# Optimization experiments

Hardware: AMD Instinct MI355X
Metric: run time of the kernel (lower is better)

The kernel has to match this reference:

```python
import jax, jax.numpy as jnp
import numpy as np

NQ = 4        # nqubits
NLAYERS = 2   # nlayers
DIM = 2 ** NQ # statevector size = 16


def _apply_1q(state, U, wire, batched):
    """Apply a single-qubit gate U on `wire` to state [B, 16].
    U is [B,2,2] if batched else [2,2]. Pennylane wire 0 = most significant bit."""
    B = state.shape[0]
    st = state.reshape((B,) + (2,) * NQ)
    ax = wire + 1
    st = jnp.moveaxis(st, ax, -1).reshape(B, DIM // 2, 2)
    if batched:
        st = jnp.einsum('bij,bkj->bki', U, st)
    else:
        st = jnp.einsum('ij,bkj->bki', U, st)
    st = st.reshape((B,) + (2,) * NQ)  # last axis is the wire axis now
    st = jnp.moveaxis(st, -1, ax)
    return st.reshape(B, DIM)


def _apply_cnot(state, c, t):
    """CNOT with control c, target t on state [B, 16]."""
    B = state.shape[0]
    st = state.reshape((B,) + (2,) * NQ)
    cax, tax = c + 1, t + 1
    s0 = jnp.take(st, 0, axis=cax)  # control=0 slice, axis removed
    s1 = jnp.take(st, 1, axis=cax)  # control=1 slice
    s1 = jnp.flip(s1, axis=tax - (1 if tax > cax else 0))  # X on target
    st = jnp.stack([s0, s1], axis=cax)
    return st.reshape(B, DIM)


def _simulate(angles, qnn_weights):
    """Batched 4-qubit circuit: RX(angles) encoding, then NLAYERS of
    [RY(weights) on each wire, CNOT ring]. Returns <Z_i> per wire: [B, 4]."""
    B = angles.shape[0]
    state = jnp.zeros((B, DIM), dtype=jnp.complex64).at[:, 0].set(1.0)

    # RX encoding (per-sample angles)
    c = jnp.cos(angles / 2)
    s = jnp.sin(angles / 2)
    for w in range(NQ):
        row0 = jnp.stack([c[:, w] + 0j, -1j * s[:, w]], axis=-1)
        row1 = jnp.stack([-1j * s[:, w], c[:, w] + 0j], axis=-1)
        U = jnp.stack([row0, row1], axis=-2)  # [B,2,2] complex64
        state = _apply_1q(state, U, w, batched=True)

    # Entangling layers (shared weights)
    cw = jnp.cos(qnn_weights / 2)
    sw = jnp.sin(qnn_weights / 2)
    for layer in range(NLAYERS):
        for w in range(NQ):
            k = w + layer * NQ
            U = jnp.stack([jnp.stack([cw[k], -sw[k]]),
                           jnp.stack([sw[k], cw[k]])]).astype(jnp.complex64)
            state = _apply_1q(state, U, w, batched=False)
        for w in range(NQ):
            state = _apply_cnot(state, w, (w + 1) % NQ)

    # <Z_i> = P(bit_i = 0) - P(bit_i = 1)
    probs = jnp.abs(state) ** 2  # [B, 16] real float32
    pr = probs.reshape((B,) + (2,) * NQ)
    evs = []
    for w in range(NQ):
        axes = tuple(a for a in range(1, NQ + 1) if a != w + 1)
        marg = pr.sum(axis=axes)  # [B, 2]
        evs.append(marg[:, 0] - marg[:, 1])
    return jnp.stack(evs, axis=-1)  # [B, 4]


def setup_inputs() -> dict:
    key = jax.random.key(0)
    ks = jax.random.split(key, 6)
    B = 131072
    x = jax.random.uniform(ks[0], (B, 28, 28), dtype=jnp.float32) * 255.0
    W_red = jax.random.normal(ks[1], (NQ, 28 * 28), dtype=jnp.float32) * 0.03
    b_red = jax.random.normal(ks[2], (NQ,), dtype=jnp.float32) * 0.01
    qnn_weights = jax.random.uniform(ks[3], (NLAYERS * NQ,), dtype=jnp.float32) * np.pi
    W_out = jax.random.normal(ks[4], (10, NQ), dtype=jnp.float32) * 0.3
    b_out = jax.random.normal(ks[5], (10,), dtype=jnp.float32) * 0.01
    return {"x": x, "W_red": W_red, "b_red": b_red,
            "qnn_weights": qnn_weights, "W_out": W_out, "b_out": b_out}


def reference(x, W_red, b_red, qnn_weights, W_out, b_out):
    B = x.shape[0]
    h = x.reshape(B, -1) / 255.0
    h = h @ W_red.T + b_red                 # [B, 4]
    angles = jnp.tanh(h) * jnp.pi           # [B, 4]
    ev = _simulate(angles, qnn_weights)     # [B, 4]
    return ev @ W_out.T + b_out             # [B, 10]
```

## Files before the change

### kernel.cpp

```cpp
#include <hip/hip_runtime.h>
#include <math.h>

#define PI_F 3.14159265358979323846f

__device__ __forceinline__ float dot4(const float4 a, const float4 b) {
    return a.x * b.x + a.y * b.y + a.z * b.z + a.w * b.w;
}

template<int P>
__device__ __forceinline__ void rx_gate(float (&ar)[16], float (&ai)[16], float c, float s) {
#pragma unroll
    for (int m = 0; m < 8; ++m) {
        const int i0 = ((m >> P) << (P + 1)) | (m & ((1 << P) - 1));
        const int i1 = i0 | (1 << P);
        const float a0r = ar[i0], a0i = ai[i0], a1r = ar[i1], a1i = ai[i1];
        ar[i0] = c * a0r + s * a1i;
        ai[i0] = c * a0i - s * a1r;
        ar[i1] = c * a1r + s * a0i;
        ai[i1] = c * a1i - s * a0r;
    }
}

template<int P>
__device__ __forceinline__ void ry_gate(float (&ar)[16], float (&ai)[16], float c, float s) {
#pragma unroll
    for (int m = 0; m < 8; ++m) {
        const int i0 = ((m >> P) << (P + 1)) | (m & ((1 << P) - 1));
        const int i1 = i0 | (1 << P);
        const float a0r = ar[i0], a0i = ai[i0], a1r = ar[i1], a1i = ai[i1];
        ar[i0] = c * a0r - s * a1r;
        ai[i0] = c * a0i - s * a1i;
        ar[i1] = s * a0r + c * a1r;
        ai[i1] = s * a0i + c * a1i;
    }
}

template<int PC, int PT>
__device__ __forceinline__ void cnot_gate(float (&ar)[16], float (&ai)[16]) {
#pragma unroll
    for (int i = 0; i < 16; ++i) {
        if ((i & (1 << PC)) && !(i & (1 << PT))) {
            const int j = i | (1 << PT);
            float tr = ar[i]; ar[i] = ar[j]; ar[j] = tr;
            float ti = ai[i]; ai[i] = ai[j]; ai[j] = ti;
        }
    }
}

__device__ __forceinline__ float pack_reduce4(int lane, float s0, float s1, float s2, float s3) {
    const bool b1 = (lane & 1) != 0;
    const bool b2 = (lane & 2) != 0;
    const float u01 = (b1 ? s1 : s0) + __shfl_xor(b1 ? s0 : s1, 1);
    const float u23 = (b1 ? s3 : s2) + __shfl_xor(b1 ? s2 : s3, 1);
    float v = (b2 ? u23 : u01) + __shfl_xor(b2 ? u01 : u23, 2);
    v += __shfl_xor(v, 4);
    v += __shfl_xor(v, 8);
    v += __shfl_xor(v, 16);
    v += __shfl_xor(v, 32);
    return v;
}

__global__ __launch_bounds__(256, 4)
void hybrid_qnn_kernel(const float* __restrict__ x,
                       const float* __restrict__ W_red,
                       const float* __restrict__ b_red,
                       const float* __restrict__ qw,
                       const float* __restrict__ W_out,
                       const float* __restrict__ b_out,
                       float* __restrict__ out,
                       int B)
{
    __shared__ float h_lds[64][4];
    __shared__ float qc_lds[8];
    __shared__ float qs_lds[8];
    __shared__ float outStage[640];

    const int t = threadIdx.x;
    const int lane = t & 63;
    const int wave = t >> 6;
    const long long blockBase = (long long)blockIdx.x * 64;
    const long long wbase = blockBase + wave * 16;

    if (t < 8) {
        const float a = 0.5f * qw[t];
        qc_lds[t] = cosf(a);
        qs_lds[t] = sinf(a);
    }

    const float inv255 = 1.0f / 255.0f;

    float4 Wl[3][4];
#pragma unroll
    for (int c = 0; c < 3; ++c) {
#pragma unroll
        for (int j = 0; j < 4; ++j) {
            const float4 w = *(const float4*)(W_red + j * 784 + 4 * (lane + 64 * c));
            Wl[c][j] = make_float4(w.x * inv255, w.y * inv255, w.z * inv255, w.w * inv255);
        }
    }
    const float br0 = b_red[0], br1 = b_red[1], br2 = b_red[2], br3 = b_red[3];

    {
        const int s = lane >> 2;
        const int c = lane & 3;
        const long long samp = wbase + s;
        float4 wt[4];
#pragma unroll
        for (int j = 0; j < 4; ++j) {
            const float4 w = *(const float4*)(W_red + j * 784 + 768 + 4 * c);
            wt[j] = make_float4(w.x * inv255, w.y * inv255, w.z * inv255, w.w * inv255);
        }
        float4 xt = make_float4(0.f, 0.f, 0.f, 0.f);
        if (samp < B) xt = *(const float4*)(x + (size_t)samp * 784 + 768 + 4 * c);
        float d0 = dot4(xt, wt[0]);
        float d1 = dot4(xt, wt[1]);
        float d2 = dot4(xt, wt[2]);
        float d3 = dot4(xt, wt[3]);
        d0 += __shfl_xor(d0, 1); d0 += __shfl_xor(d0, 2);
        d1 += __shfl_xor(d1, 1); d1 += __shfl_xor(d1, 2);
        d2 += __shfl_xor(d2, 1); d2 += __shfl_xor(d2, 2);
        d3 += __shfl_xor(d3, 1); d3 += __shfl_xor(d3, 2);
        if (c == 0 && samp < B) {
            const int srow = wave * 16 + s;
            h_lds[srow][0] = d0 + br0;
            h_lds[srow][1] = d1 + br1;
            h_lds[srow][2] = d2 + br2;
            h_lds[srow][3] = d3 + br3;
        }
    }

    if (wbase + 16 <= B) {
        const float* xbase = x + (size_t)wbase * 784;
        float4 a0 = *(const float4*)(xbase + 4 * lane);
        float4 a1 = *(const float4*)(xbase + 4 * (lane + 64));
        float4 a2 = *(const float4*)(xbase + 4 * (lane + 128));
        float4 b0 = *(const float4*)(xbase + 784 + 4 * lane);
        float4 b1 = *(const float4*)(xbase + 784 + 4 * (lane + 64));
        float4 b2 = *(const float4*)(xbase + 784 + 4 * (lane + 128));
#pragma unroll
        for (int q = 0; q < 16; ++q) {
            const float4 x0 = a0, x1 = a1, x2 = a2;
            a0 = b0; a1 = b1; a2 = b2;
            if (q + 2 < 16) {
                const float* nb = xbase + (size_t)(q + 2) * 784;
                b0 = *(const float4*)(nb + 4 * lane);
                b1 = *(const float4*)(nb + 4 * (lane + 64));
                b2 = *(const float4*)(nb + 4 * (lane + 128));
            }
            const float s0 = dot4(x0, Wl[0][0]) + dot4(x1, Wl[1][0]) + dot4(x2, Wl[2][0]);
            const float s1 = dot4(x0, Wl[0][1]) + dot4(x1, Wl[1][1]) + dot4(x2, Wl[2][1]);
            const float s2 = dot4(x0, Wl[0][2]) + dot4(x1, Wl[1][2]) + dot4(x2, Wl[2][2]);
            const float s3 = dot4(x0, Wl[0][3]) + dot4(x1, Wl[1][3]) + dot4(x2, Wl[2][3]);
            const float v = pack_reduce4(lane, s0, s1, s2, s3);
            if (lane < 4) h_lds[wave * 16 + q][lane] += v;
        }
    } else {
        for (int q = 0; q < 16; ++q) {
            const long long samp = wbase + q;
            if (samp >= B) break;
            const float* xb = x + (size_t)samp * 784;
            const float4 x0 = *(const float4*)(xb + 4 * lane);
            const float4 x1 = *(const float4*)(xb + 4 * (lane + 64));
            const float4 x2 = *(const float4*)(xb + 4 * (lane + 128));
            const float s0 = dot4(x0, Wl[0][0]) + dot4(x1, Wl[1][0]) + dot4(x2, Wl[2][0]);
            const float s1 = dot4(x0, Wl[0][1]) + dot4(x1, Wl[1][1]) + dot4(x2, Wl[2][1]);
            const float s2 = dot4(x0, Wl[0][2]) + dot4(x1, Wl[1][2]) + dot4(x2, Wl[2][2]);
            const float s3 = dot4(x0, Wl[0][3]) + dot4(x1, Wl[1][3]) + dot4(x2, Wl[2][3]);
            const float v = pack_reduce4(lane, s0, s1, s2, s3);
            if (lane < 4) h_lds[wave * 16 + q][lane] += v;
        }
    }
    __syncthreads();

    if (t < 64 && blockBase + t < B) {
        const float ang0 = tanhf(h_lds[t][0]) * PI_F;
        const float ang1 = tanhf(h_lds[t][1]) * PI_F;
        const float ang2 = tanhf(h_lds[t][2]) * PI_F;
        const float ang3 = tanhf(h_lds[t][3]) * PI_F;
        const float c0 = cosf(0.5f * ang0), sn0 = sinf(0.5f * ang0);
        const float c1 = cosf(0.5f * ang1), sn1 = sinf(0.5f * ang1);
        const float c2 = cosf(0.5f * ang2), sn2 = sinf(0.5f * ang2);
        const float c3 = cosf(0.5f * ang3), sn3 = sinf(0.5f * ang3);

        float ar[16], ai[16];
#pragma unroll
        for (int i = 0; i < 16; ++i) { ar[i] = 0.f; ai[i] = 0.f; }
        ar[0] = 1.f;

        rx_gate<3>(ar, ai, c0, sn0);
        rx_gate<2>(ar, ai, c1, sn1);
        rx_gate<1>(ar, ai, c2, sn2);
        rx_gate<0>(ar, ai, c3, sn3);

#pragma unroll
        for (int layer = 0; layer < 2; ++layer) {
            const int k0 = layer * 4;
            ry_gate<3>(ar, ai, qc_lds[k0 + 0], qs_lds[k0 + 0]);
            ry_gate<2>(ar, ai, qc_lds[k0 + 1], qs_lds[k0 + 1]);
            ry_gate<1>(ar, ai, qc_lds[k0 + 2], qs_lds[k0 + 2]);
            ry_gate<0>(ar, ai, qc_lds[k0 + 3], qs_lds[k0 + 3]);
            cnot_gate<3, 2>(ar, ai);
            cnot_gate<2, 1>(ar, ai);
            cnot_gate<1, 0>(ar, ai);
            cnot_gate<0, 3>(ar, ai);
        }

        float pr[16];
#pragma unroll
        for (int i = 0; i < 16; ++i) pr[i] = ar[i] * ar[i] + ai[i] * ai[i];

        float ev[4];
#pragma unroll
        for (int w = 0; w < 4; ++w) {
            const int p = 3 - w;
            float e = 0.f;
#pragma unroll
            for (int i = 0; i < 16; ++i) e += (i & (1 << p)) ? -pr[i] : pr[i];
            ev[w] = e;
        }

#pragma unroll
        for (int n = 0; n < 10; ++n) {
            float o = b_out[n];
#pragma unroll
            for (int j = 0; j < 4; ++j) o += ev[j] * W_out[n * 4 + j];
            outStage[t * 10 + n] = o;
        }
    }
    __syncthreads();

    const long long outBase = (long long)blockIdx.x * 640;
    const long long outTotal = (long long)B * 10;
#pragma unroll
    for (int i = t; i < 640; i += 256) {
        const long long oi = outBase + i;
        if (oi < outTotal) out[oi] = outStage[i];
    }
}

extern "C" void kernel_launch(void* const* d_in, const int* in_sizes, int n_in,
                              void* d_out, int out_size, void* d_ws, size_t ws_size,
                              hipStream_t stream) {
    const float* x      = (const float*)d_in[0];
    const float* W_red  = (const float*)d_in[1];
    const float* b_red  = (const float*)d_in[2];
    const float* qw     = (const float*)d_in[3];
    const float* W_out  = (const float*)d_in[4];
    const float* b_out  = (const float*)d_in[5];
    float* out = (float*)d_out;

    const int B = in_sizes[0] / 784;
    const int grid = (B + 63) / 64;
    hipLaunchKernelGGL(hybrid_qnn_kernel, dim3(grid), dim3(256), 0, stream,
                       x, W_red, b_red, qw, W_out, b_out, out, B);
}
```

Measured before the change: 80.78 us.

## Split GEMV and quantum simulation into two kernels via workspace

Splits the single fused kernel in two. The first computes the 4-wide projection h and writes it to a workspace buffer. The second runs the statevector simulation with all 256 threads per block active, where before only 64 threads per block did the serial simulation tail. The aim is to stop 3 of 4 waves idling during the simulation phase, at the cost of an extra launch and a small global round trip for h. The fused path is kept as a fallback when no workspace is available.

```diff
diff --git a/kernel.cpp b/kernel.cpp
--- a/kernel.cpp
+++ b/kernel.cpp
@@ -60,32 +60,81 @@
     return v;
 }
 
+__device__ __forceinline__ void sim_and_project(
+    float h0, float h1, float h2, float h3,
+    const float* qc, const float* qs,
+    const float* __restrict__ W_out, const float* __restrict__ b_out,
+    float* outRow )
+{
+    const float ang0 = tanhf(h0) * PI_F;
+    const float ang1 = tanhf(h1) * PI_F;
+    const float ang2 = tanhf(h2) * PI_F;
+    const float ang3 = tanhf(h3) * PI_F;
+    const float c0 = cosf(0.5f * ang0), sn0 = sinf(0.5f * ang0);
+    const float c1 = cosf(0.5f * ang1), sn1 = sinf(0.5f * ang1);
+    const float c2 = cosf(0.5f * ang2), sn2 = sinf(0.5f * ang2);
+    const float c3 = cosf(0.5f * ang3), sn3 = sinf(0.5f * ang3);
+
+    float ar[16], ai[16];
+#pragma unroll
+    for (int i = 0; i < 16; ++i) { ar[i] = 0.f; ai[i] = 0.f; }
+    ar[0] = 1.f;
+
+    rx_gate<3>(ar, ai, c0, sn0);
+    rx_gate<2>(ar, ai, c1, sn1);
+    rx_gate<1>(ar, ai, c2, sn2);
+    rx_gate<0>(ar, ai, c3, sn3);
+
+#pragma unroll
+    for (int layer = 0; layer < 2; ++layer) {
+        const int k0 = layer * 4;
+        ry_gate<3>(ar, ai, qc[k0 + 0], qs[k0 + 0]);
+        ry_gate<2>(ar, ai, qc[k0 + 1], qs[k0 + 1]);
+        ry_gate<1>(ar, ai, qc[k0 + 2], qs[k0 + 2]);
+        ry_gate<0>(ar, ai, qc[k0 + 3], qs[k0 + 3]);
+        cnot_gate<3, 2>(ar, ai);
+        cnot_gate<2, 1>(ar, ai);
+        cnot_gate<1, 0>(ar, ai);
+        cnot_gate<0, 3>(ar, ai);
+    }
+
+    float pr[16];
+#pragma unroll
+    for (int i = 0; i < 16; ++i) pr[i] = ar[i] * ar[i] + ai[i] * ai[i];
+
+    float ev[4];
+#pragma unroll
+    for (int w = 0; w < 4; ++w) {
+        const int p = 3 - w;
+        float e = 0.f;
+#pragma unroll
+        for (int i = 0; i < 16; ++i) e += (i & (1 << p)) ? -pr[i] : pr[i];
+        ev[w] = e;
+    }
+
+#pragma unroll
+    for (int n = 0; n < 10; ++n) {
+        float o = b_out[n];
+#pragma unroll
+        for (int j = 0; j < 4; ++j) o += ev[j] * W_out[n * 4 + j];
+        outRow[n] = o;
+    }
+}
+
 __global__ __launch_bounds__(256, 4)
-void hybrid_qnn_kernel(const float* __restrict__ x,
-                       const float* __restrict__ W_red,
-                       const float* __restrict__ b_red,
-                       const float* __restrict__ qw,
-                       const float* __restrict__ W_out,
-                       const float* __restrict__ b_out,
-                       float* __restrict__ out,
-                       int B)
+void gemm_h_kernel(const float* __restrict__ x,
+                   const float* __restrict__ W_red,
+                   const float* __restrict__ b_red,
+                   float* __restrict__ hws,
+                   int B)
 {
     __shared__ float h_lds[64][4];
-    __shared__ float qc_lds[8];
-    __shared__ float qs_lds[8];
-    __shared__ float outStage[640];
 
     const int t = threadIdx.x;
     const int lane = t & 63;
     const int wave = t >> 6;
     const long long blockBase = (long long)blockIdx.x * 64;
     const long long wbase = blockBase + wave * 16;
-
-    if (t < 8) {
-        const float a = 0.5f * qw[t];
-        qc_lds[t] = cosf(a);
-        qs_lds[t] = sinf(a);
-    }
 
     const float inv255 = 1.0f / 255.0f;
 
@@ -172,60 +221,167 @@
     }
     __syncthreads();
 
+    const long long hb = blockBase * 4;
+    const long long samp = blockBase + (t >> 2);
+    if (samp < B) hws[hb + t] = ((const float*)h_lds)[t];
+}
+
+__global__ __launch_bounds__(256, 4)
+void sim_out_kernel(const float* __restrict__ hws,
+                    const float* __restrict__ qw,
+                    const float* __restrict__ W_out,
+                    const float* __restrict__ b_out,
+                    float* __restrict__ out,
+                    int B)
+{
+    __shared__ float qc_lds[8];
+    __shared__ float qs_lds[8];
+    __shared__ float outStage[2560];
+
+    const int t = threadIdx.x;
+    if (t < 8) {
+        const float a = 0.5f * qw[t];
+        qc_lds[t] = cosf(a);
+        qs_lds[t] = sinf(a);
+    }
+    __syncthreads();
+
+    const long long s = (long long)blockIdx.x * 256 + t;
+    if (s < B) {
+        const float4 h = *(const float4*)(hws + 4 * s);
+        float row[10];
+        sim_and_project(h.x, h.y, h.z, h.w, qc_lds, qs_lds, W_out, b_out, row);
+#pragma unroll
+        for (int n = 0; n < 10; ++n) outStage[t * 10 + n] = row[n];
+    }
+    __syncthreads();
+
+    const long long ob = (long long)blockIdx.x * 2560;
+    const long long outTotal = (long long)B * 10;
+#pragma unroll
+    for (int i = t; i < 2560; i += 256) {
+        const long long oi = ob + i;
+        if (oi < outTotal) out[oi] = outStage[i];
+    }
+}
+
+__global__ __launch_bounds__(256, 4)
+void hybrid_qnn_fused_kernel(const float* __restrict__ x,
+                             const float* __restrict__ W_red,
+                             const float* __restrict__ b_red,
+                             const float* __restrict__ qw,
+                             const float* __restrict__ W_out,
+                             const float* __restrict__ b_out,
+                             float* __restrict__ out,
+                             int B)
+{
+    __shared__ float h_lds[64][4];
+    __shared__ float qc_lds[8];
+    __shared__ float qs_lds[8];
+    __shared__ float outStage[640];
+
+    const int t = threadIdx.x;
+    const int lane = t & 63;
+    const int wave = t >> 6;
+    const long long blockBase = (long long)blockIdx.x * 64;
+    const long long wbase = blockBase + wave * 16;
+
+    if (t < 8) {
+        const float a = 0.5f * qw[t];
+        qc_lds[t] = cosf(a);
+        qs_lds[t] = sinf(a);
+    }
+
+    const float inv255 = 1.0f / 255.0f;
+    float4 Wl[3][4];
+#pragma unroll
+    for (int c = 0; c < 3; ++c) {
+#pragma unroll
+        for (int j = 0; j < 4; ++j) {
+            const float4 w = *(const float4*)(W_red + j * 784 + 4 * (lane + 64 * c));
+            Wl[c][j] = make_float4(w.x * inv255, w.y * inv255, w.z * inv255, w.w * inv255);
+        }
+    }
+    const float br0 = b_red[0], br1 = b_red[1], br2 = b_red[2], br3 = b_red[3];
+
+    {
+        const int s = lane >> 2;
+        const int c = lane & 3;
+        const long long samp = wbase + s;
+        float4 wt[4];
+#pragma unroll
+        for (int j = 0; j < 4; ++j) {
+            const float4 w = *(const float4*)(W_red + j * 784 + 768 + 4 * c);
+            wt[j] = make_float4(w.x * inv255, w.y * inv255, w.z * inv255, w.w * inv255);
+        }
+        float4 xt = make_float4(0.f, 0.f, 0.f, 0.f);
+        if (samp < B) xt = *(const float4*)(x + (size_t)samp * 784 + 768 + 4 * c);
+        float d0 = dot4(xt, wt[0]);
+        float d1 = dot4(xt, wt[1]);
+        float d2 = dot4(xt, wt[2]);
+        float d3 = dot4(xt, wt[3]);
+        d0 += __shfl_xor(d0, 1); d0 += __shfl_xor(d0, 2);
+        d1 += __shfl_xor(d1, 1); d1 += __shfl_xor(d1, 2);
+        d2 += __shfl_xor(d2, 1); d2 += __shfl_xor(d2, 2);
+        d3 += __shfl_xor(d3, 1); d3 += __shfl_xor(d3, 2);
+        if (c == 0 && samp < B) {
+            const int srow = wave * 16 + s;
+            h_lds[srow][0] = d0 + br0;
+            h_lds[srow][1] = d1 + br1;
+            h_lds[srow][2] = d2 + br2;
+            h_lds[srow][3] = d3 + br3;
+        }
+    }
+
+    if (wbase + 16 <= B) {
+        const float* xbase = x + (size_t)wbase * 784;
+        float4 a0 = *(const float4*)(xbase + 4 * lane);
+        float4 a1 = *(const float4*)(xbase + 4 * (lane + 64));
+        float4 a2 = *(const float4*)(xbase + 4 * (lane + 128));
+        float4 b0 = *(const float4*)(xbase + 784 + 4 * lane);
+        float4 b1 = *(const float4*)(xbase + 784 + 4 * (lane + 64));
+        float4 b2 = *(const float4*)(xbase + 784 + 4 * (lane + 128));
+#pragma unroll
+        for (int q = 0; q < 16; ++q) {
+            const float4 x0 = a0, x1 = a1, x2 = a2;
+            a0 = b0; a1 = b1; a2 = b2;
+            if (q + 2 < 16) {
+                const float* nb = xbase + (size_t)(q + 2) * 784;
+                b0 = *(const float4*)(nb + 4 * lane);
+                b1 = *(const float4*)(nb + 4 * (lane + 64));
+                b2 = *(const float4*)(nb + 4 * (lane + 128));
+            }
+            const float s0 = dot4(x0, Wl[0][0]) + dot4(x1, Wl[1][0]) + dot4(x2, Wl[2][0]);
+            const float s1 = dot4(x0, Wl[0][1]) + dot4(x1, Wl[1][1]) + dot4(x2, Wl[2][1]);
+            const float s2 = dot4(x0, Wl[0][2]) + dot4(x1, Wl[1][2]) + dot4(x2, Wl[2][2]);
+            const float s3 = dot4(x0, Wl[0][3]) + dot4(x1, Wl[1][3]) + dot4(x2, Wl[2][3]);
+            const float v = pack_reduce4(lane, s0, s1, s2, s3);
+            if (lane < 4) h_lds[wave * 16 + q][lane] += v;
+        }
+    } else {
+        for (int q = 0; q < 16; ++q) {
+            const long long samp = wbase + q;
+            if (samp >= B) break;
+            const float* xb = x + (size_t)samp * 784;
+            const float4 x0 = *(const float4*)(xb + 4 * lane);
+            const float4 x1 = *(const float4*)(xb + 4 * (lane + 64));
+            const float4 x2 = *(const float4*)(xb + 4 * (lane + 128));
+            const float s0 = dot4(x0, Wl[0][0]) + dot4(x1, Wl[1][0]) + dot4(x2, Wl[2][0]);
+            const float s1 = dot4(x0, Wl[0][1]) + dot4(x1, Wl[1][1]) + dot4(x2, Wl[2][1]);
+            const float s2 = dot4(x0, Wl[0][2]) + dot4(x1, Wl[1][2]) + dot4(x2, Wl[2][2]);
+            const float s3 = dot4(x0, Wl[0][3]) + dot4(x1, Wl[1][3]) + dot4(x2, Wl[2][3]);
+            const float v = pack_reduce4(lane, s0, s1, s2, s3);
+            if (lane < 4) h_lds[wave * 16 + q][lane] += v;
+        }
+    }
+    __syncthreads();
+
     if (t < 64 && blockBase + t < B) {
-        const float ang0 = tanhf(h_lds[t][0]) * PI_F;
-        const float ang1 = tanhf(h_lds[t][1]) * PI_F;
-        const float ang2 = tanhf(h_lds[t][2]) * PI_F;
-        const float ang3 = tanhf(h_lds[t][3]) * PI_F;
-        const float c0 = cosf(0.5f * ang0), sn0 = sinf(0.5f * ang0);
-        const float c1 = cosf(0.5f * ang1), sn1 = sinf(0.5f * ang1);
-        const float c2 = cosf(0.5f * ang2), sn2 = sinf(0.5f * ang2);
-        const float c3 = cosf(0.5f * ang3), sn3 = sinf(0.5f * ang3);
-
-        float ar[16], ai[16];
-#pragma unroll
-        for (int i = 0; i < 16; ++i) { ar[i] = 0.f; ai[i] = 0.f; }
-        ar[0] = 1.f;
-
-        rx_gate<3>(ar, ai, c0, sn0);
-        rx_gate<2>(ar, ai, c1, sn1);
-        rx_gate<1>(ar, ai, c2, sn2);
-        rx_gate<0>(ar, ai, c3, sn3);
-
-#pragma unroll
-        for (int layer = 0; layer < 2; ++layer) {
-            const int k0 = layer * 4;
-            ry_gate<3>(ar, ai, qc_lds[k0 + 0], qs_lds[k0 + 0]);
-            ry_gate<2>(ar, ai, qc_lds[k0 + 1], qs_lds[k0 + 1]);
-            ry_gate<1>(ar, ai, qc_lds[k0 + 2], qs_lds[k0 + 2]);
-            ry_gate<0>(ar, ai, qc_lds[k0 + 3], qs_lds[k0 + 3]);
-            cnot_gate<3, 2>(ar, ai);
-            cnot_gate<2, 1>(ar, ai);
-            cnot_gate<1, 0>(ar, ai);
-            cnot_gate<0, 3>(ar, ai);
-        }
-
-        float pr[16];
-#pragma unroll
-        for (int i = 0; i < 16; ++i) pr[i] = ar[i] * ar[i] + ai[i] * ai[i];
-
-        float ev[4];
-#pragma unroll
-        for (int w = 0; w < 4; ++w) {
-            const int p = 3 - w;
-            float e = 0.f;
-#pragma unroll
-            for (int i = 0; i < 16; ++i) e += (i & (1 << p)) ? -pr[i] : pr[i];
-            ev[w] = e;
-        }
-
-#pragma unroll
-        for (int n = 0; n < 10; ++n) {
-            float o = b_out[n];
-#pragma unroll
-            for (int j = 0; j < 4; ++j) o += ev[j] * W_out[n * 4 + j];
-            outStage[t * 10 + n] = o;
-        }
+        float row[10];
+        sim_and_project(h_lds[t][0], h_lds[t][1], h_lds[t][2], h_lds[t][3],
+                        qc_lds, qs_lds, W_out, b_out, row);
+#pragma unroll
+        for (int n = 0; n < 10; ++n) outStage[t * 10 + n] = row[n];
     }
     __syncthreads();
 
@@ -250,7 +406,19 @@
     float* out = (float*)d_out;
 
     const int B = in_sizes[0] / 784;
-    const int grid = (B + 63) / 64;
-    hipLaunchKernelGGL(hybrid_qnn_kernel, dim3(grid), dim3(256), 0, stream,
-                       x, W_red, b_red, qw, W_out, b_out, out, B);
-}
+    const size_t hBytes = (size_t)B * 4 * sizeof(float);
+
+    if (ws_size >= hBytes && d_ws != nullptr) {
+        float* hws = (float*)d_ws;
+        const int grid1 = (B + 63) / 64;
+        hipLaunchKernelGGL(gemm_h_kernel, dim3(grid1), dim3(256), 0, stream,
+                           x, W_red, b_red, hws, B);
+        const int grid2 = (B + 255) / 256;
+        hipLaunchKernelGGL(sim_out_kernel, dim3(grid2), dim3(256), 0, stream,
+                           hws, qw, W_out, b_out, out, B);
+    } else {
+        const int grid = (B + 63) / 64;
+        hipLaunchKernelGGL(hybrid_qnn_fused_kernel, dim3(grid), dim3(256), 0, stream,
+                           x, W_red, b_red, qw, W_out, b_out, out, B);
+    }
+}
```

Result: slower. 85.27 us (+5.6%).
